# Performance work log

Measured on AMD Instinct MI355X. Metric: run time of the kernel, lower is better.

## Reference

```python
import jax, jax.numpy as jnp
import numpy as np
from jax import lax

IN_CH = 256
UP = 8
DN = ('NCHW', 'OIHW', 'NCHW')


def setup_inputs() -> dict:
    key = jax.random.key(0)
    ks = jax.random.split(key, 6)
    B, H, W = 8, 96, 96
    flow_lr = jax.random.normal(ks[0], (B, 2, H, W), dtype=jnp.float32)
    feat = jax.random.normal(ks[1], (B, IN_CH, H, W), dtype=jnp.float32)
    w1 = jax.random.normal(ks[2], (IN_CH, IN_CH, 3, 3), dtype=jnp.float32) * 0.02
    b1 = jnp.zeros((IN_CH,), dtype=jnp.float32)
    w2 = jax.random.normal(ks[3], (UP * UP * 9, IN_CH, 1, 1), dtype=jnp.float32) * 0.02
    b2 = jnp.zeros((UP * UP * 9,), dtype=jnp.float32)
    return {"flow_lr": flow_lr, "feat": feat, "w1": w1, "b1": b1, "w2": w2, "b2": b2}


def reference(flow_lr, feat, w1, b1, w2, b2):
    B, _, H, W = flow_lr.shape
    up = UP
    # mask head: 3x3 conv + relu + 1x1 conv
    x = lax.conv_general_dilated(feat, w1, (1, 1), 'SAME', dimension_numbers=DN)
    x = jax.nn.relu(x + b1[None, :, None, None])
    mask = lax.conv_general_dilated(x, w2, (1, 1), 'SAME', dimension_numbers=DN)
    mask = mask + b2[None, :, None, None]
    # channel dim 9*up*up splits as (9, up, up), matching torch .view(B,1,9,up,up,H,W)
    mask = mask.reshape(B, 9, up, up, H, W)
    mask = jax.nn.softmax(mask, axis=1)
    # unfold(flow_lr, 3, padding=1): 9 zero-padded 3x3 shifts, row-major (kh, kw)
    pad = jnp.pad(flow_lr, ((0, 0), (0, 0), (1, 1), (1, 1)))
    flow_unf = jnp.stack(
        [pad[:, :, i:i + H, j:j + W] for i in range(3) for j in range(3)], axis=2
    )  # (B, 2, 9, H, W)
    # convex combination over the 9 neighbors
    up_flow = jnp.einsum('bkpqhw,bckhw->bcpqhw', mask, flow_unf)  # (B,2,up,up,H,W)
    # pixel-shuffle: (B,2,p,q,H,W) -> (B,2,H,p,W,q) -> (B,2,H*up,W*up)
    up_flow = up_flow.transpose(0, 1, 4, 2, 5, 3).reshape(B, 2, H * up, W * up)
    return up_flow * up
```

## Files before the change

### kernel.cpp

```cpp
#include <hip/hip_runtime.h>
#include <hip/hip_bf16.h>
#include <stdint.h>

typedef unsigned short u16;
typedef __bf16 bf16x8 __attribute__((ext_vector_type(8)));
typedef float f32x4 __attribute__((ext_vector_type(4)));

#define MFMA16(a, b, c) __builtin_amdgcn_mfma_f32_16x16x32_bf16((a), (b), (c), 0, 0, 0)

#define GLOAD16(g, l)                                                        \
  __builtin_amdgcn_global_load_lds(                                          \
      (const __attribute__((address_space(1))) void*)(g),                    \
      (__attribute__((address_space(3))) void*)(l), 16, 0, 0)

static __device__ __forceinline__ u16 f2bf(float f) {
  union { float f; uint32_t u; } v;
  v.f = f;
  uint32_t u = v.u;
  return (u16)((u + 0x7FFFu + ((u >> 16) & 1u)) >> 16);
}
static __device__ __forceinline__ float u2f(uint32_t u) {
  union { uint32_t u; float f; } v;
  v.u = u;
  return v.f;
}

#define FEATT_ELEMS (8u * 98u * 98u * 256u)
#define W1T_OFF     FEATT_ELEMS
#define W1T_ELEMS   (256u * 2304u)
#define W2B_OFF     (W1T_OFF + W1T_ELEMS)
#define W2B_ELEMS   (576u * 256u)
#define X_OFF       (W2B_OFF + W2B_ELEMS)

__global__ __launch_bounds__(256) void halo_zero(u16* __restrict__ featT) {
  int tid = blockIdx.x * 256 + threadIdx.x;
  int b = tid / (388 * 32);
  int rem = tid % (388 * 32);
  int pos = rem >> 5, v = rem & 31;
  int h, w;
  if (pos < 98) { h = 0; w = pos; }
  else if (pos < 196) { h = 97; w = pos - 98; }
  else if (pos < 292) { h = pos - 196 + 1; w = 0; }
  else { h = pos - 292 + 1; w = 97; }
  uint4* dst = (uint4*)(featT + (size_t)((b * 98 + h) * 98 + w) * 256 + v * 8);
  *dst = make_uint4(0, 0, 0, 0);
}

__global__ __launch_bounds__(256) void prep_featT(const float* __restrict__ feat,
                                                  u16* __restrict__ featT) {
  const int pt = blockIdx.x, ct = blockIdx.y, b = blockIdx.z;
  const int p0 = pt * 64, c0 = ct * 64;
  __shared__ float tile[64][65];
  const int t = threadIdx.x;
  const int pj = t & 63, ci0 = t >> 6;
#pragma unroll
  for (int r = 0; r < 16; ++r) {
    int ci = r * 4 + ci0;
    tile[ci][pj] = feat[(b * 256 + c0 + ci) * 9216 + p0 + pj];
  }
  __syncthreads();
  const int pl = t >> 2, cc0 = (t & 3) * 16;
  const int pix = p0 + pl;
  const int h = pix / 96, w = pix % 96;
  uint32_t u[8];
#pragma unroll
  for (int i = 0; i < 8; ++i) {
    u16 lo = f2bf(tile[cc0 + 2 * i][pl]);
    u16 hi = f2bf(tile[cc0 + 2 * i + 1][pl]);
    u[i] = (uint32_t)lo | ((uint32_t)hi << 16);
  }
  uint4* dst = (uint4*)(featT + (size_t)((b * 98 + h + 1) * 98 + (w + 1)) * 256 + c0 + cc0);
  dst[0] = make_uint4(u[0], u[1], u[2], u[3]);
  dst[1] = make_uint4(u[4], u[5], u[6], u[7]);
}

__global__ __launch_bounds__(256) void prep_w(const float* __restrict__ w1,
                                              const float* __restrict__ w2,
                                              u16* __restrict__ w1t,
                                              u16* __restrict__ w2b) {
  int i = blockIdx.x * 256 + threadIdx.x;
  if (i < 589824) {
    int oc = i / 2304, r = i % 2304;
    int tap = r >> 8, cin = r & 255;
    w1t[i] = f2bf(w1[(oc * 256 + cin) * 9 + tap]);
  } else {
    int j = i - 589824;
    if (j < 147456) w2b[j] = f2bf(w2[j]);
  }
}

__global__ __launch_bounds__(512, 4) void gemm1(const u16* __restrict__ featT,
                                                const u16* __restrict__ w1t,
                                                const float* __restrict__ b1,
                                                u16* __restrict__ xout) {
  __shared__ __align__(16) u16 sA[128 * 64];
  __shared__ __align__(16) u16 sB[256 * 64];
  __shared__ float sb1[256];

  const int t = threadIdx.x;
  const int wave = t >> 6, lane = t & 63;
  const int mt = blockIdx.x;
  const int b = mt / 72;
  const int ip0 = (mt % 72) * 128;

  if (t < 256) sb1[t] = b1[t];

  const u16* aBase[2];
  const u16* bBase[4];
#pragma unroll
  for (int r = 0; r < 2; ++r) {
    int row = r * 64 + wave * 8 + (lane >> 3);
    int chunk = (lane & 7) ^ (row & 7);
    int ip = ip0 + row;
    int h = ip / 96, w = ip % 96;
    aBase[r] = featT + (size_t)((b * 98 + h + 1) * 98 + (w + 1)) * 256 + chunk * 8;
  }
#pragma unroll
  for (int r = 0; r < 4; ++r) {
    int row = wave * 32 + r * 8 + (lane >> 3);
    int chunk = (lane & 7) ^ (row & 7);
    bBase[r] = w1t + (size_t)row * 2304 + chunk * 8;
  }

  const int wm = wave >> 2, wn = wave & 3;
  int aoffs[4][2], boffs[4][2];
#pragma unroll
  for (int m = 0; m < 4; ++m) {
#pragma unroll
    for (int ki = 0; ki < 2; ++ki) {
      int kc = ki * 4 + (lane >> 4);
      int rowa = wm * 64 + m * 16 + (lane & 15);
      aoffs[m][ki] = rowa * 64 + ((kc ^ (rowa & 7)) * 8);
      int rowb = wn * 64 + m * 16 + (lane & 15);
      boffs[m][ki] = rowb * 64 + ((kc ^ (rowb & 7)) * 8);
    }
  }

  f32x4 acc[4][4];
#pragma unroll
  for (int m = 0; m < 4; ++m)
#pragma unroll
    for (int n = 0; n < 4; ++n) acc[m][n] = f32x4{0.f, 0.f, 0.f, 0.f};

  for (int kt = 0; kt < 36; ++kt) {
    int tap = kt >> 2;
    int dh = tap / 3 - 1, dw = tap % 3 - 1;
    int aoff = (dh * 98 + dw) * 256 + (kt & 3) * 64;
    int boff = kt * 64;
#pragma unroll
    for (int r = 0; r < 2; ++r) GLOAD16(aBase[r] + aoff, &sA[(r * 64 + wave * 8) * 64]);
#pragma unroll
    for (int r = 0; r < 4; ++r) GLOAD16(bBase[r] + boff, &sB[(wave * 32 + r * 8) * 64]);
    __syncthreads();
#pragma unroll
    for (int ki = 0; ki < 2; ++ki) {
      bf16x8 av[4], bv[4];
#pragma unroll
      for (int m = 0; m < 4; ++m) av[m] = *(const bf16x8*)&sA[aoffs[m][ki]];
#pragma unroll
      for (int n = 0; n < 4; ++n) bv[n] = *(const bf16x8*)&sB[boffs[n][ki]];
#pragma unroll
      for (int m = 0; m < 4; ++m)
#pragma unroll
        for (int n = 0; n < 4; ++n) acc[m][n] = MFMA16(av[m], bv[n], acc[m][n]);
    }
    __syncthreads();
  }

  const int pix0g = mt * 128;
#pragma unroll
  for (int m = 0; m < 4; ++m) {
    int pixl = wm * 64 + m * 16 + ((lane >> 4) << 2);
#pragma unroll
    for (int n = 0; n < 4; ++n) {
      int oc = wn * 64 + n * 16 + (lane & 15);
      float bias = sb1[oc];
      f32x4 v = acc[m][n];
#pragma unroll
      for (int j = 0; j < 4; ++j) {
        float val = v[j] + bias;
        val = val > 0.f ? val : 0.f;
        xout[(size_t)(pix0g + pixl + j) * 256 + oc] = f2bf(val);
      }
    }
  }
}

__global__ __launch_bounds__(512) void gemm2f(const u16* __restrict__ xws,
                                              const u16* __restrict__ w2b,
                                              const float* __restrict__ b2g,
                                              const float* __restrict__ flow,
                                              float* __restrict__ out) {
  __shared__ __align__(16) u16 sW[18432];
  __shared__ uint32_t sFlowP[1152];
  __shared__ float sb2f[576];

  const int t = threadIdx.x;
  const int wave = t >> 6, lane = t & 63;
  const int bid = blockIdx.x;
  const int mt = (bid & 7) * 72 + (bid >> 3);
  const int b = mt / 72;
  const int ipl0 = (mt % 72) * 128;
  const int l15 = lane & 15, kc = lane >> 4;

  auto stageW = [&](int cI, int kh) {
#pragma unroll
    for (int pass = 0; pass < 5; ++pass) {
      if (pass < 4 || t < 256) {
        int c = pass * 512 + t;
        int n = c >> 4, cl = c & 15;
        int cg = cl ^ (n & 15);
        int chan = (n >> 4) * 64 + cI * 16 + (n & 15);
        GLOAD16(w2b + (size_t)chan * 256 + kh * 128 + cg * 8,
                &sW[(pass * 512 + wave * 64) * 8]);
      }
    }
  };
  stageW(0, 0);

  for (int i = t; i < 1152; i += 512) {
    int nf = i >> 7, p = i & 127;
    int ip = ipl0 + p;
    int h = ip / 96, w = ip % 96;
    int hh = h + nf / 3 - 1, ww = w + nf % 3 - 1;
    float vx = 0.f, vy = 0.f;
    if (hh >= 0 && hh < 96 && ww >= 0 && ww < 96) {
      vx = flow[b * 18432 + hh * 96 + ww];
      vy = flow[b * 18432 + 9216 + hh * 96 + ww];
    }
    sFlowP[i] = (uint32_t)f2bf(vx) | ((uint32_t)f2bf(vy) << 16);
  }
  for (int i = t; i < 576; i += 512) sb2f[i] = b2g[i];

  const int px = wave * 16 + l15;
  const u16* xr = &xws[((size_t)mt * 128 + px) * 256];
  bf16x8 areg[8];
#pragma unroll
  for (int s = 0; s < 8; ++s) areg[s] = *(const bf16x8*)&xr[(s * 4 + kc) * 8];

  const int iph = (ipl0 + px) / 96, ipw = (ipl0 + px) % 96;
  const size_t ob = ((size_t)(b * 2) * 768 + iph * 8) * 768 + ipw * 8;
  const int q0 = (kc & 1) * 4, pk = kc >> 1;

  __syncthreads();

  uint32_t fp[9];
#pragma unroll
  for (int nf = 0; nf < 9; ++nf) fp[nf] = sFlowP[nf * 128 + px];

  f32x4 acc[9];
  for (int cI = 0; cI < 4; ++cI) {
#pragma unroll
    for (int kh = 0; kh < 2; ++kh) {
      if (kh == 0) {
#pragma unroll
        for (int nf = 0; nf < 9; ++nf) acc[nf] = f32x4{0.f, 0.f, 0.f, 0.f};
      }
      __builtin_amdgcn_s_setprio(1);
#pragma unroll
      for (int ks = 0; ks < 4; ++ks) {
        bf16x8 a = areg[kh * 4 + ks];
        int kcc = ks * 4 + kc;
#pragma unroll
        for (int nf = 0; nf < 9; ++nf) {
          int n = nf * 16 + l15;
          bf16x8 wv = *(const bf16x8*)&sW[n * 128 + ((kcc ^ (n & 15)) * 8)];
          acc[nf] = MFMA16(wv, a, acc[nf]);
        }
      }
      __builtin_amdgcn_s_setprio(0);
      __syncthreads();
      if (!(cI == 3 && kh == 1)) stageW(cI + kh, kh ^ 1);

      if (kh == 1) {
        f32x4 vx4, vy4;
#pragma unroll
        for (int j = 0; j < 4; ++j) {
          int pql = kc * 4 + j;
          float v[9], mx = -3.0e38f;
#pragma unroll
          for (int nf = 0; nf < 9; ++nf) {
            v[nf] = acc[nf][j] + sb2f[nf * 64 + cI * 16 + pql];
            mx = fmaxf(mx, v[nf]);
          }
          float ssum = 0.f, fx = 0.f, fy = 0.f;
#pragma unroll
          for (int nf = 0; nf < 9; ++nf) {
            float e = __expf(v[nf] - mx);
            ssum += e;
            fx += e * u2f(fp[nf] << 16);
            fy += e * u2f(fp[nf] & 0xFFFF0000u);
          }
          float sc = 8.0f / ssum;
          vx4[j] = fx * sc;
          vy4[j] = fy * sc;
        }
        int p = cI * 2 + pk;
        *(f32x4*)&out[ob + (size_t)p * 768 + q0] = vx4;
        *(f32x4*)&out[ob + 589824 + (size_t)p * 768 + q0] = vy4;
      }
      __syncthreads();
    }
  }
}

extern "C" void kernel_launch(void* const* d_in, const int* in_sizes, int n_in,
                              void* d_out, int out_size, void* d_ws, size_t ws_size,
                              hipStream_t stream) {
  const float* flow = (const float*)d_in[0];
  const float* feat = (const float*)d_in[1];
  const float* w1 = (const float*)d_in[2];
  const float* b1 = (const float*)d_in[3];
  const float* w2 = (const float*)d_in[4];
  const float* b2 = (const float*)d_in[5];
  float* out = (float*)d_out;
  u16* ws = (u16*)d_ws;
  u16* featT = ws;
  u16* w1t = ws + W1T_OFF;
  u16* w2b = ws + W2B_OFF;
  u16* xws = ws + X_OFF;

  halo_zero<<<388, 256, 0, stream>>>(featT);
  prep_featT<<<dim3(144, 4, 8), 256, 0, stream>>>(feat, featT);
  prep_w<<<2880, 256, 0, stream>>>(w1, w2, w1t, w2b);
  gemm1<<<576, 512, 0, stream>>>(featT, w1t, b1, xws);
  gemm2f<<<576, 512, 0, stream>>>(xws, w2b, b2, flow, out);
}
```

Baseline: 194.2 us.

## Double-buffer W2 staging in quarter-K steps with one barrier per step

The fused 1x1-conv/softmax/upsample kernel now splits each output-channel group's K dimension into four 64-wide chunks instead of two 128-wide halves. The W2 tiles go into two alternating LDS buffers. The next chunk is prefetched right after a single barrier, so the loads overlap the MFMAs on the current buffer, replacing the earlier single-buffer scheme that needed two barriers per step. The XOR swizzle is narrowed to 8 groups to match the smaller tile. The trade-off is more, smaller load rounds and a fully unrolled 16-step loop, which may raise code size and register pressure.

```diff
diff --git a/kernel.cpp b/kernel.cpp
--- a/kernel.cpp
+++ b/kernel.cpp
@@ -186,12 +186,12 @@
   }
 }
 
-__global__ __launch_bounds__(512) void gemm2f(const u16* __restrict__ xws,
-                                              const u16* __restrict__ w2b,
-                                              const float* __restrict__ b2g,
-                                              const float* __restrict__ flow,
-                                              float* __restrict__ out) {
-  __shared__ __align__(16) u16 sW[18432];
+__global__ __launch_bounds__(512) void gemm2fq(const u16* __restrict__ xws,
+                                               const u16* __restrict__ w2b,
+                                               const float* __restrict__ b2g,
+                                               const float* __restrict__ flow,
+                                               float* __restrict__ out) {
+  __shared__ __align__(16) u16 sW[2][9216];
   __shared__ uint32_t sFlowP[1152];
   __shared__ float sb2f[576];
 
@@ -203,20 +203,21 @@
   const int ipl0 = (mt % 72) * 128;
   const int l15 = lane & 15, kc = lane >> 4;
 
-  auto stageW = [&](int cI, int kh) {
-#pragma unroll
-    for (int pass = 0; pass < 5; ++pass) {
-      if (pass < 4 || t < 256) {
-        int c = pass * 512 + t;
-        int n = c >> 4, cl = c & 15;
-        int cg = cl ^ (n & 15);
+  auto stageQ = [&](int u, int bufi) {
+    int cI = u >> 2, kq = u & 3;
+    if (t < 384) {
+#pragma unroll
+      for (int pass = 0; pass < 3; ++pass) {
+        int c = pass * 384 + t;
+        int n = c >> 3, cl = c & 7;
+        int cg = cl ^ (n & 7);
         int chan = (n >> 4) * 64 + cI * 16 + (n & 15);
-        GLOAD16(w2b + (size_t)chan * 256 + kh * 128 + cg * 8,
-                &sW[(pass * 512 + wave * 64) * 8]);
+        GLOAD16(w2b + (size_t)chan * 256 + kq * 64 + cg * 8,
+                &sW[bufi][(pass * 384 + wave * 64) * 8]);
       }
     }
   };
-  stageW(0, 0);
+  stageQ(0, 0);
 
   for (int i = t; i < 1152; i += 512) {
     int nf = i >> 7, p = i & 127;
@@ -242,64 +243,61 @@
   const size_t ob = ((size_t)(b * 2) * 768 + iph * 8) * 768 + ipw * 8;
   const int q0 = (kc & 1) * 4, pk = kc >> 1;
 
-  __syncthreads();
-
   uint32_t fp[9];
-#pragma unroll
-  for (int nf = 0; nf < 9; ++nf) fp[nf] = sFlowP[nf * 128 + px];
-
   f32x4 acc[9];
-  for (int cI = 0; cI < 4; ++cI) {
-#pragma unroll
-    for (int kh = 0; kh < 2; ++kh) {
-      if (kh == 0) {
-#pragma unroll
-        for (int nf = 0; nf < 9; ++nf) acc[nf] = f32x4{0.f, 0.f, 0.f, 0.f};
+#pragma unroll
+  for (int u = 0; u < 16; ++u) {
+    __syncthreads();
+    if (u == 0) {
+#pragma unroll
+      for (int nf = 0; nf < 9; ++nf) fp[nf] = sFlowP[nf * 128 + px];
+    }
+    if (u < 15) stageQ(u + 1, (u + 1) & 1);
+    const int cI = u >> 2, kq = u & 3;
+    if (kq == 0) {
+#pragma unroll
+      for (int nf = 0; nf < 9; ++nf) acc[nf] = f32x4{0.f, 0.f, 0.f, 0.f};
+    }
+    const u16* base = sW[u & 1];
+    __builtin_amdgcn_s_setprio(1);
+#pragma unroll
+    for (int ki = 0; ki < 2; ++ki) {
+      bf16x8 a = areg[kq * 2 + ki];
+      int kcc = ki * 4 + kc;
+#pragma unroll
+      for (int nf = 0; nf < 9; ++nf) {
+        int n = nf * 16 + l15;
+        bf16x8 wv = *(const bf16x8*)&base[n * 64 + ((kcc ^ (n & 7)) * 8)];
+        acc[nf] = MFMA16(wv, a, acc[nf]);
       }
-      __builtin_amdgcn_s_setprio(1);
-#pragma unroll
-      for (int ks = 0; ks < 4; ++ks) {
-        bf16x8 a = areg[kh * 4 + ks];
-        int kcc = ks * 4 + kc;
+    }
+    __builtin_amdgcn_s_setprio(0);
+    if (kq == 3) {
+      f32x4 vx4, vy4;
+#pragma unroll
+      for (int j = 0; j < 4; ++j) {
+        int pql = kc * 4 + j;
+        float v[9], mx = -3.0e38f;
 #pragma unroll
         for (int nf = 0; nf < 9; ++nf) {
-          int n = nf * 16 + l15;
-          bf16x8 wv = *(const bf16x8*)&sW[n * 128 + ((kcc ^ (n & 15)) * 8)];
-          acc[nf] = MFMA16(wv, a, acc[nf]);
+          v[nf] = acc[nf][j] + sb2f[nf * 64 + cI * 16 + pql];
+          mx = fmaxf(mx, v[nf]);
         }
+        float ssum = 0.f, fx = 0.f, fy = 0.f;
+#pragma unroll
+        for (int nf = 0; nf < 9; ++nf) {
+          float e = __expf(v[nf] - mx);
+          ssum += e;
+          fx += e * u2f(fp[nf] << 16);
+          fy += e * u2f(fp[nf] & 0xFFFF0000u);
+        }
+        float sc = 8.0f / ssum;
+        vx4[j] = fx * sc;
+        vy4[j] = fy * sc;
       }
-      __builtin_amdgcn_s_setprio(0);
-      __syncthreads();
-      if (!(cI == 3 && kh == 1)) stageW(cI + kh, kh ^ 1);
-
-      if (kh == 1) {
-        f32x4 vx4, vy4;
-#pragma unroll
-        for (int j = 0; j < 4; ++j) {
-          int pql = kc * 4 + j;
-          float v[9], mx = -3.0e38f;
-#pragma unroll
-          for (int nf = 0; nf < 9; ++nf) {
-            v[nf] = acc[nf][j] + sb2f[nf * 64 + cI * 16 + pql];
-            mx = fmaxf(mx, v[nf]);
-          }
-          float ssum = 0.f, fx = 0.f, fy = 0.f;
-#pragma unroll
-          for (int nf = 0; nf < 9; ++nf) {
-            float e = __expf(v[nf] - mx);
-            ssum += e;
-            fx += e * u2f(fp[nf] << 16);
-            fy += e * u2f(fp[nf] & 0xFFFF0000u);
-          }
-          float sc = 8.0f / ssum;
-          vx4[j] = fx * sc;
-          vy4[j] = fy * sc;
-        }
-        int p = cI * 2 + pk;
-        *(f32x4*)&out[ob + (size_t)p * 768 + q0] = vx4;
-        *(f32x4*)&out[ob + 589824 + (size_t)p * 768 + q0] = vy4;
-      }
-      __syncthreads();
+      int p = cI * 2 + pk;
+      *(f32x4*)&out[ob + (size_t)p * 768 + q0] = vx4;
+      *(f32x4*)&out[ob + 589824 + (size_t)p * 768 + q0] = vy4;
     }
   }
 }
@@ -324,5 +322,5 @@
   prep_featT<<<dim3(144, 4, 8), 256, 0, stream>>>(feat, featT);
   prep_w<<<2880, 256, 0, stream>>>(w1, w2, w1t, w2b);
   gemm1<<<576, 512, 0, stream>>>(featT, w1t, b1, xws);
-  gemm2f<<<576, 512, 0, stream>>>(xws, w2b, b2, flow, out);
-}
+  gemm2fq<<<576, 512, 0, stream>>>(xws, w2b, b2, flow, out);
+}
```

Result: no change. 193.3 us (-0.4%).
